# Performance work log

Measured on AMD Instinct MI355X. Metric: run time of the kernel, lower is better.

The kernel has to match this reference:

```python
import jax, jax.numpy as jnp
import numpy as np

BATCH, IN_DIM, UNITS = 65536, 256, 512

def _mask(in_dim, out_dim, density, seed):
    rng = np.random.default_rng(seed)
    return jnp.asarray((rng.random((in_dim, out_dim)) < density).astype(np.float32))

def setup_inputs() -> dict:
    key = jax.random.key(0)
    ks = jax.random.split(key, 16)
    d = {"x": jax.random.normal(ks[0], (BATCH, IN_DIM), dtype=jnp.float32)}
    # layer 0
    d["W0"] = jax.random.normal(ks[1], (IN_DIM, UNITS), dtype=jnp.float32) * 0.05
    d["b0"] = jnp.zeros((UNITS,), dtype=jnp.float32)
    d["M0"] = _mask(IN_DIM, UNITS, 0.10, 42 + 0)
    d["f0"], d["a0"], d["d0"] = jnp.float32(1.0), jnp.float32(1.0), jnp.float32(0.1)
    # layer 1 (+ skip from inputs)
    d["W1"] = jax.random.normal(ks[2], (UNITS, UNITS), dtype=jnp.float32) * 0.05
    d["b1"] = jnp.zeros((UNITS,), dtype=jnp.float32)
    d["M1"] = _mask(UNITS, UNITS, 0.10, 42 + 1)
    d["f1"], d["a1"], d["d1"] = jnp.float32(1.5), jnp.float32(1.0), jnp.float32(0.1)
    d["S1"] = jax.random.normal(ks[3], (IN_DIM, UNITS), dtype=jnp.float32) * 0.05
    d["SM1"] = _mask(IN_DIM, UNITS, 0.05, 200 + 1)
    # layer 2 (+ skip from inputs)
    d["W2"] = jax.random.normal(ks[4], (UNITS, UNITS), dtype=jnp.float32) * 0.05
    d["b2"] = jnp.zeros((UNITS,), dtype=jnp.float32)
    d["M2"] = _mask(UNITS, UNITS, 0.10, 42 + 2)
    d["f2"], d["a2"], d["d2"] = jnp.float32(2.0), jnp.float32(1.0), jnp.float32(0.1)
    d["S2"] = jax.random.normal(ks[5], (IN_DIM, UNITS), dtype=jnp.float32) * 0.05
    d["SM2"] = _mask(IN_DIM, UNITS, 0.05, 200 + 2)
    return d

def _sine(z, f, a, dec):
    # ParametricSineActivation: amplitude * sin(frequency*z) * exp(-decay*|z|)
    return a * jnp.sin(f * z) * jnp.exp(-dec * jnp.abs(z))

def reference(x, W0, b0, M0, f0, a0, d0,
              W1, b1, M1, f1, a1, d1, S1, SM1,
              W2, b2, M2, f2, a2, d2, S2, SM2):
    h0 = _sine(x @ (W0 * M0) + b0, f0, a0, d0)                       # [B, U]
    h1 = _sine(h0 @ (W1 * M1) + b1, f1, a1, d1) + x @ (S1 * SM1)     # [B, U]
    h2 = _sine(h1 @ (W2 * M2) + b2, f2, a2, d2) + x @ (S2 * SM2)     # [B, U]
    return jnp.concatenate([h0, h1, h2], axis=-1)                    # [B, 3U]
```

## Files before the change

kernel.cpp:

```cpp
#include <hip/hip_runtime.h>


#define IN_DIM 256
#define UNITS  512
#define OUTC   1536

typedef __bf16 bf16x8 __attribute__((ext_vector_type(8)));
typedef unsigned short us8 __attribute__((ext_vector_type(8)));
typedef unsigned short us4 __attribute__((ext_vector_type(4)));
typedef float f32x4 __attribute__((ext_vector_type(4)));

#define W0OFF 0
#define W1OFF 131072
#define W2OFF 393216
#define S1OFF 655360
#define S2OFF 786432

__device__ __forceinline__ unsigned short f2bf(float f) {
    unsigned u = __float_as_uint(f);
    u += 0x7FFFu + ((u >> 16) & 1u);
    return (unsigned short)(u >> 16);
}

__global__ __launch_bounds__(256) void prep_weights(
    const float* __restrict__ W0, const float* __restrict__ M0,
    const float* __restrict__ W1, const float* __restrict__ M1,
    const float* __restrict__ W2, const float* __restrict__ M2,
    const float* __restrict__ S1, const float* __restrict__ SM1,
    const float* __restrict__ S2, const float* __restrict__ SM2,
    unsigned short* __restrict__ ws)
{
    int g = blockIdx.x * 256 + threadIdx.x;
    const float* W; const float* M; int obase; int q;
    if (g < 16384)      { W = W0; M = M0;  obase = W0OFF; q = g; }
    else if (g < 49152) { W = W1; M = M1;  obase = W1OFF; q = g - 16384; }
    else if (g < 81920) { W = W2; M = M2;  obase = W2OFF; q = g - 49152; }
    else if (g < 98304) { W = S1; M = SM1; obase = S1OFF; q = g - 81920; }
    else                { W = S2; M = SM2; obase = S2OFF; q = g - 98304; }
    int frag = q >> 6, lane = q & 63;
    int kf = frag >> 5, nb = frag & 31;
    int k0 = kf * 32 + (lane >> 4) * 8;
    int n  = nb * 16 + (lane & 15);
    us8 o;
#pragma unroll
    for (int i = 0; i < 8; ++i) {
        size_t idx = (size_t)(k0 + i) * UNITS + n;
        o[i] = f2bf(W[idx] * M[idx]);
    }
    *(us8*)(ws + obase + (size_t)q * 8) = o;
}

template<int KF, int PITCH>
__device__ __forceinline__ void mm_acc(f32x4 (&acc)[2][4],
    const unsigned char* __restrict__ lsrc,
    const unsigned short* __restrict__ wfrag,
    int lane)
{
    const int lcol = lane & 15, lhi = lane >> 4;

    us8 bcur[4]; bf16x8 acur[2];
#pragma unroll
    for (int c = 0; c < 4; ++c)
        bcur[c] = *(const us8*)(wfrag + (size_t)((0 * 32 + c) * 64 + lane) * 8);
#pragma unroll
    for (int r = 0; r < 2; ++r) {
        int row = r * 16 + lcol;
        unsigned off = ((unsigned)(row * PITCH + (0 + lhi * 8) * 2)) ^ ((unsigned)((row & 7) << 4));
        acur[r] = __builtin_bit_cast(bf16x8, *(const us8*)(lsrc + off));
    }

#pragma unroll
    for (int kf = 0; kf < KF; ++kf) {
        us8 bnxt[4]; bf16x8 anxt[2];
        if (kf + 1 < KF) {
#pragma unroll
            for (int c = 0; c < 4; ++c)
                bnxt[c] = *(const us8*)(wfrag + (size_t)(((kf + 1) * 32 + c) * 64 + lane) * 8);
#pragma unroll
            for (int r = 0; r < 2; ++r) {
                int row = r * 16 + lcol;
                unsigned off = ((unsigned)(row * PITCH + ((kf + 1) * 32 + lhi * 8) * 2))
                             ^ ((unsigned)((row & 7) << 4));
                anxt[r] = __builtin_bit_cast(bf16x8, *(const us8*)(lsrc + off));
            }
        }
#pragma unroll
        for (int c = 0; c < 4; ++c) {
            bf16x8 b = __builtin_bit_cast(bf16x8, bcur[c]);
#pragma unroll
            for (int r = 0; r < 2; ++r)
                acc[r][c] = __builtin_amdgcn_mfma_f32_16x16x32_bf16(acur[r], b, acc[r][c], 0, 0, 0);
        }
        if (kf + 1 < KF) {
#pragma unroll
            for (int c = 0; c < 4; ++c) bcur[c] = bnxt[c];
#pragma unroll
            for (int r = 0; r < 2; ++r) acur[r] = anxt[r];
        }
    }
}

__device__ __forceinline__ void writeout(const unsigned char* __restrict__ hs,
                                         float* __restrict__ dst, long rb, int t)
{
    int row = t >> 4, c0 = (t & 15) * 32;
    float* o = dst + (rb + row) * OUTC + c0;
    unsigned base = (unsigned)(row * 1024 + c0 * 2);
    unsigned swz  = (unsigned)((row & 7) << 4);
#pragma unroll
    for (int i = 0; i < 4; ++i) {
        us8 v = *(const us8*)(hs + ((base + (unsigned)i * 16) ^ swz));
        f32x4 lo, hi;
#pragma unroll
        for (int j = 0; j < 4; ++j) {
            lo[j] = __uint_as_float((unsigned)v[j] << 16);
            hi[j] = __uint_as_float((unsigned)v[j + 4] << 16);
        }
        *(f32x4*)(o + i * 8)     = lo;
        *(f32x4*)(o + i * 8 + 4) = hi;
    }
}

__global__ __launch_bounds__(512, 4) void reservoir_main(
    const float* __restrict__ x,
    const unsigned short* __restrict__ wb,
    const float* __restrict__ b0, const float* __restrict__ b1, const float* __restrict__ b2,
    const float* __restrict__ pf0, const float* __restrict__ pa0, const float* __restrict__ pd0,
    const float* __restrict__ pf1, const float* __restrict__ pa1, const float* __restrict__ pd1,
    const float* __restrict__ pf2, const float* __restrict__ pa2, const float* __restrict__ pd2,
    float* __restrict__ out)
{
    __shared__ __align__(16) unsigned char lds[49152];
    unsigned char* xs = lds;
    unsigned char* hs = lds + 16384;

    const int t = threadIdx.x;
    const int wave = t >> 6, lane = t & 63;
    const int lcol = lane & 15, lhi = lane >> 4;
    const long rb = (long)blockIdx.x * 32;
    const int cb = wave * 64;
    const unsigned nb0e = (unsigned)(wave * 4) * 512;

    const float f0v = pf0[0], a0v = pa0[0], d0v = pd0[0];
    const float f1v = pf1[0], a1v = pa1[0], d1v = pd1[0];
    const float f2v = pf2[0], a2v = pa2[0], d2v = pd2[0];

    {
        int r  = t >> 4;
        int cq = (t & 15) * 4;
        const float* xp = x + (rb + r) * IN_DIM + cq;
        unsigned base = (unsigned)(r * 512 + cq * 2);
        unsigned swz  = (unsigned)((r & 7) << 4);
#pragma unroll
        for (int j = 0; j < 4; ++j) {
            f32x4 v = *(const f32x4*)(xp + j * 64);
            us4 h;
            h[0] = f2bf(v[0]); h[1] = f2bf(v[1]); h[2] = f2bf(v[2]); h[3] = f2bf(v[3]);
            *(us4*)(xs + ((base + (unsigned)j * 128) ^ swz)) = h;
        }
    }
    __syncthreads();

    f32x4 acc[2][4];

#pragma unroll
    for (int r = 0; r < 2; ++r)
#pragma unroll
        for (int c = 0; c < 4; ++c) acc[r][c] = (f32x4){0.f, 0.f, 0.f, 0.f};

    mm_acc<8, 512>(acc, xs, wb + W0OFF + nb0e, lane);

    {
        float bias[4];
#pragma unroll
        for (int c = 0; c < 4; ++c) bias[c] = b0[cb + c * 16 + lcol];
#pragma unroll
        for (int r = 0; r < 2; ++r) {
#pragma unroll
            for (int j = 0; j < 4; ++j) {
                int row = r * 16 + lhi * 4 + j;
                unsigned hswz = (unsigned)((row & 7) << 4);
#pragma unroll
                for (int c = 0; c < 4; ++c) {
                    int col = cb + c * 16 + lcol;
                    float z = acc[r][c][j] + bias[c];
                    float h = a0v * __sinf(f0v * z) * __expf(-d0v * fabsf(z));
                    *(unsigned short*)(hs + (((unsigned)(row * 1024 + col * 2)) ^ hswz)) = f2bf(h);
                }
            }
        }
    }
    __syncthreads();

    writeout(hs, out, rb, t);

#pragma unroll
    for (int r = 0; r < 2; ++r)
#pragma unroll
        for (int c = 0; c < 4; ++c) acc[r][c] = (f32x4){0.f, 0.f, 0.f, 0.f};

    mm_acc<16, 1024>(acc, hs, wb + W1OFF + nb0e, lane);

    {
        float bias[4];
#pragma unroll
        for (int c = 0; c < 4; ++c) bias[c] = b1[cb + c * 16 + lcol];
#pragma unroll
        for (int c = 0; c < 4; ++c) {
#pragma unroll
            for (int r = 0; r < 2; ++r) {
#pragma unroll
                for (int j = 0; j < 4; ++j) {
                    float z = acc[r][c][j] + bias[c];
                    acc[r][c][j] = a1v * __sinf(f1v * z) * __expf(-d1v * fabsf(z));
                }
            }
        }
    }
    mm_acc<8, 512>(acc, xs, wb + S1OFF + nb0e, lane);
    __syncthreads();

#pragma unroll
    for (int r = 0; r < 2; ++r) {
#pragma unroll
        for (int j = 0; j < 4; ++j) {
            int row = r * 16 + lhi * 4 + j;
            unsigned hswz = (unsigned)((row & 7) << 4);
#pragma unroll
            for (int c = 0; c < 4; ++c) {
                int col = cb + c * 16 + lcol;
                *(unsigned short*)(hs + (((unsigned)(row * 1024 + col * 2)) ^ hswz)) = f2bf(acc[r][c][j]);
            }
        }
    }
    __syncthreads();

    writeout(hs, out + UNITS, rb, t);

#pragma unroll
    for (int r = 0; r < 2; ++r)
#pragma unroll
        for (int c = 0; c < 4; ++c) acc[r][c] = (f32x4){0.f, 0.f, 0.f, 0.f};

    mm_acc<16, 1024>(acc, hs, wb + W2OFF + nb0e, lane);

    {
        float bias[4];
#pragma unroll
        for (int c = 0; c < 4; ++c) bias[c] = b2[cb + c * 16 + lcol];
#pragma unroll
        for (int c = 0; c < 4; ++c) {
#pragma unroll
            for (int r = 0; r < 2; ++r) {
#pragma unroll
                for (int j = 0; j < 4; ++j) {
                    float z = acc[r][c][j] + bias[c];
                    acc[r][c][j] = a2v * __sinf(f2v * z) * __expf(-d2v * fabsf(z));
                }
            }
        }
    }
    mm_acc<8, 512>(acc, xs, wb + S2OFF + nb0e, lane);
    __syncthreads();

#pragma unroll
    for (int r = 0; r < 2; ++r) {
#pragma unroll
        for (int j = 0; j < 4; ++j) {
            int row = r * 16 + lhi * 4 + j;
            unsigned hswz = (unsigned)((row & 7) << 4);
#pragma unroll
            for (int c = 0; c < 4; ++c) {
                int col = cb + c * 16 + lcol;
                *(unsigned short*)(hs + (((unsigned)(row * 1024 + col * 2)) ^ hswz)) = f2bf(acc[r][c][j]);
            }
        }
    }
    __syncthreads();

    writeout(hs, out + 2 * UNITS, rb, t);
}

extern "C" void kernel_launch(void* const* d_in, const int* in_sizes, int n_in,
                              void* d_out, int out_size, void* d_ws, size_t ws_size,
                              hipStream_t stream)
{
    (void)in_sizes; (void)n_in; (void)out_size; (void)ws_size;
    const float* x   = (const float*)d_in[0];
    const float* W0  = (const float*)d_in[1];
    const float* b0  = (const float*)d_in[2];
    const float* M0  = (const float*)d_in[3];
    const float* f0  = (const float*)d_in[4];
    const float* a0  = (const float*)d_in[5];
    const float* d0  = (const float*)d_in[6];
    const float* W1  = (const float*)d_in[7];
    const float* b1  = (const float*)d_in[8];
    const float* M1  = (const float*)d_in[9];
    const float* f1  = (const float*)d_in[10];
    const float* a1  = (const float*)d_in[11];
    const float* d1  = (const float*)d_in[12];
    const float* S1  = (const float*)d_in[13];
    const float* SM1 = (const float*)d_in[14];
    const float* W2  = (const float*)d_in[15];
    const float* b2  = (const float*)d_in[16];
    const float* M2  = (const float*)d_in[17];
    const float* f2  = (const float*)d_in[18];
    const float* a2  = (const float*)d_in[19];
    const float* d2  = (const float*)d_in[20];
    const float* S2  = (const float*)d_in[21];
    const float* SM2 = (const float*)d_in[22];

    unsigned short* wb = (unsigned short*)d_ws;
    float* out = (float*)d_out;

    prep_weights<<<448, 256, 0, stream>>>(W0, M0, W1, M1, W2, M2, S1, SM1, S2, SM2, wb);
    reservoir_main<<<65536 / 32, 512, 0, stream>>>(x, wb, b0, b1, b2,
                                                   f0, a0, d0, f1, a1, d1, f2, a2, d2, out);
}
```

Before: 769.0 us.

## Double row tile to 64 per block and deepen fragment prefetch to two stages

Each block now processes 64 batch rows instead of 32. Each wave accumulates a 4x4 grid of MFMA tiles, so every weight fragment loaded from global memory feeds twice as many MFMAs, which halves weight traffic per row. The k-loop prefetch is deepened from one to two stages to hide load latency. In exchange, LDS use doubles to 96KB, accumulator registers double, and launch bounds drop to 2 blocks per CU, which lowers occupancy and halves the grid size.

```diff
diff --git a/kernel.cpp b/kernel.cpp
--- a/kernel.cpp
+++ b/kernel.cpp
@@ -51,77 +51,71 @@
 }
 
 template<int KF, int PITCH>
-__device__ __forceinline__ void mm_acc(f32x4 (&acc)[2][4],
+__device__ __forceinline__ void mm_acc(f32x4 (&acc)[4][4],
     const unsigned char* __restrict__ lsrc,
     const unsigned short* __restrict__ wfrag,
     int lane)
 {
     const int lcol = lane & 15, lhi = lane >> 4;
 
-    us8 bcur[4]; bf16x8 acur[2];
-#pragma unroll
-    for (int c = 0; c < 4; ++c)
-        bcur[c] = *(const us8*)(wfrag + (size_t)((0 * 32 + c) * 64 + lane) * 8);
-#pragma unroll
-    for (int r = 0; r < 2; ++r) {
-        int row = r * 16 + lcol;
-        unsigned off = ((unsigned)(row * PITCH + (0 + lhi * 8) * 2)) ^ ((unsigned)((row & 7) << 4));
-        acur[r] = __builtin_bit_cast(bf16x8, *(const us8*)(lsrc + off));
-    }
+#define LOADB(dst, kk) { _Pragma("unroll") \
+    for (int c_ = 0; c_ < 4; ++c_) \
+        dst[c_] = *(const us8*)(wfrag + (size_t)(((kk) * 32 + c_) * 64 + lane) * 8); }
+#define LOADA(dst, kk) { _Pragma("unroll") \
+    for (int r_ = 0; r_ < 4; ++r_) { \
+        int row_ = r_ * 16 + lcol; \
+        unsigned off_ = ((unsigned)(row_ * PITCH + ((kk) * 32 + lhi * 8) * 2)) \
+                      ^ ((unsigned)((row_ & 7) << 4)); \
+        dst[r_] = __builtin_bit_cast(bf16x8, *(const us8*)(lsrc + off_)); } }
+
+    us8 bc[4], bn[4]; bf16x8 ac[4], an[4];
+    LOADB(bc, 0); LOADA(ac, 0);
+    if (KF > 1) { LOADB(bn, 1); LOADA(an, 1); }
 
 #pragma unroll
     for (int kf = 0; kf < KF; ++kf) {
-        us8 bnxt[4]; bf16x8 anxt[2];
-        if (kf + 1 < KF) {
-#pragma unroll
-            for (int c = 0; c < 4; ++c)
-                bnxt[c] = *(const us8*)(wfrag + (size_t)(((kf + 1) * 32 + c) * 64 + lane) * 8);
-#pragma unroll
-            for (int r = 0; r < 2; ++r) {
-                int row = r * 16 + lcol;
-                unsigned off = ((unsigned)(row * PITCH + ((kf + 1) * 32 + lhi * 8) * 2))
-                             ^ ((unsigned)((row & 7) << 4));
-                anxt[r] = __builtin_bit_cast(bf16x8, *(const us8*)(lsrc + off));
-            }
-        }
+        us8 bf_[4]; bf16x8 af_[4];
+        if (kf + 2 < KF) { LOADB(bf_, kf + 2); LOADA(af_, kf + 2); }
 #pragma unroll
         for (int c = 0; c < 4; ++c) {
-            bf16x8 b = __builtin_bit_cast(bf16x8, bcur[c]);
-#pragma unroll
-            for (int r = 0; r < 2; ++r)
-                acc[r][c] = __builtin_amdgcn_mfma_f32_16x16x32_bf16(acur[r], b, acc[r][c], 0, 0, 0);
-        }
-        if (kf + 1 < KF) {
-#pragma unroll
-            for (int c = 0; c < 4; ++c) bcur[c] = bnxt[c];
-#pragma unroll
-            for (int r = 0; r < 2; ++r) acur[r] = anxt[r];
-        }
-    }
+            bf16x8 b = __builtin_bit_cast(bf16x8, bc[c]);
+#pragma unroll
+            for (int r = 0; r < 4; ++r)
+                acc[r][c] = __builtin_amdgcn_mfma_f32_16x16x32_bf16(ac[r], b, acc[r][c], 0, 0, 0);
+        }
+#pragma unroll
+        for (int i = 0; i < 4; ++i) { bc[i] = bn[i]; ac[i] = an[i]; bn[i] = bf_[i]; an[i] = af_[i]; }
+    }
+#undef LOADB
+#undef LOADA
 }
 
 __device__ __forceinline__ void writeout(const unsigned char* __restrict__ hs,
                                          float* __restrict__ dst, long rb, int t)
 {
-    int row = t >> 4, c0 = (t & 15) * 32;
-    float* o = dst + (rb + row) * OUTC + c0;
-    unsigned base = (unsigned)(row * 1024 + c0 * 2);
-    unsigned swz  = (unsigned)((row & 7) << 4);
-#pragma unroll
-    for (int i = 0; i < 4; ++i) {
-        us8 v = *(const us8*)(hs + ((base + (unsigned)i * 16) ^ swz));
-        f32x4 lo, hi;
-#pragma unroll
-        for (int j = 0; j < 4; ++j) {
-            lo[j] = __uint_as_float((unsigned)v[j] << 16);
-            hi[j] = __uint_as_float((unsigned)v[j + 4] << 16);
-        }
-        *(f32x4*)(o + i * 8)     = lo;
-        *(f32x4*)(o + i * 8 + 4) = hi;
-    }
-}
-
-__global__ __launch_bounds__(512, 4) void reservoir_main(
+#pragma unroll
+    for (int half = 0; half < 2; ++half) {
+        int row = (t >> 4) + half * 32;
+        int c0 = (t & 15) * 32;
+        float* o = dst + (rb + row) * OUTC + c0;
+        unsigned base = (unsigned)(row * 1024 + c0 * 2);
+        unsigned swz  = (unsigned)((row & 7) << 4);
+#pragma unroll
+        for (int i = 0; i < 4; ++i) {
+            us8 v = *(const us8*)(hs + ((base + (unsigned)i * 16) ^ swz));
+            f32x4 lo, hi;
+#pragma unroll
+            for (int j = 0; j < 4; ++j) {
+                lo[j] = __uint_as_float((unsigned)v[j] << 16);
+                hi[j] = __uint_as_float((unsigned)v[j + 4] << 16);
+            }
+            *(f32x4*)(o + i * 8)     = lo;
+            *(f32x4*)(o + i * 8 + 4) = hi;
+        }
+    }
+}
+
+__global__ __launch_bounds__(512, 2) void reservoir_main(
     const float* __restrict__ x,
     const unsigned short* __restrict__ wb,
     const float* __restrict__ b0, const float* __restrict__ b1, const float* __restrict__ b2,
@@ -130,14 +124,14 @@
     const float* __restrict__ pf2, const float* __restrict__ pa2, const float* __restrict__ pd2,
     float* __restrict__ out)
 {
-    __shared__ __align__(16) unsigned char lds[49152];
+    __shared__ __align__(16) unsigned char lds[98304];
     unsigned char* xs = lds;
-    unsigned char* hs = lds + 16384;
+    unsigned char* hs = lds + 32768;
 
     const int t = threadIdx.x;
     const int wave = t >> 6, lane = t & 63;
     const int lcol = lane & 15, lhi = lane >> 4;
-    const long rb = (long)blockIdx.x * 32;
+    const long rb = (long)blockIdx.x * 64;
     const int cb = wave * 64;
     const unsigned nb0e = (unsigned)(wave * 4) * 512;
 
@@ -146,25 +140,25 @@
     const float f2v = pf2[0], a2v = pa2[0], d2v = pd2[0];
 
     {
-        int r  = t >> 4;
-        int cq = (t & 15) * 4;
+        int r  = t >> 3;
+        int cq = (t & 7) * 4;
         const float* xp = x + (rb + r) * IN_DIM + cq;
         unsigned base = (unsigned)(r * 512 + cq * 2);
         unsigned swz  = (unsigned)((r & 7) << 4);
 #pragma unroll
-        for (int j = 0; j < 4; ++j) {
-            f32x4 v = *(const f32x4*)(xp + j * 64);
+        for (int j = 0; j < 8; ++j) {
+            f32x4 v = *(const f32x4*)(xp + j * 32);
             us4 h;
             h[0] = f2bf(v[0]); h[1] = f2bf(v[1]); h[2] = f2bf(v[2]); h[3] = f2bf(v[3]);
-            *(us4*)(xs + ((base + (unsigned)j * 128) ^ swz)) = h;
-        }
-    }
-    __syncthreads();
-
-    f32x4 acc[2][4];
-
-#pragma unroll
-    for (int r = 0; r < 2; ++r)
+            *(us4*)(xs + ((base + (unsigned)j * 64) ^ swz)) = h;
+        }
+    }
+    __syncthreads();
+
+    f32x4 acc[4][4];
+
+#pragma unroll
+    for (int r = 0; r < 4; ++r)
 #pragma unroll
         for (int c = 0; c < 4; ++c) acc[r][c] = (f32x4){0.f, 0.f, 0.f, 0.f};
 
@@ -175,7 +169,7 @@
 #pragma unroll
         for (int c = 0; c < 4; ++c) bias[c] = b0[cb + c * 16 + lcol];
 #pragma unroll
-        for (int r = 0; r < 2; ++r) {
+        for (int r = 0; r < 4; ++r) {
 #pragma unroll
             for (int j = 0; j < 4; ++j) {
                 int row = r * 16 + lhi * 4 + j;
@@ -195,7 +189,7 @@
     writeout(hs, out, rb, t);
 
 #pragma unroll
-    for (int r = 0; r < 2; ++r)
+    for (int r = 0; r < 4; ++r)
 #pragma unroll
         for (int c = 0; c < 4; ++c) acc[r][c] = (f32x4){0.f, 0.f, 0.f, 0.f};
 
@@ -208,7 +202,7 @@
 #pragma unroll
         for (int c = 0; c < 4; ++c) {
 #pragma unroll
-            for (int r = 0; r < 2; ++r) {
+            for (int r = 0; r < 4; ++r) {
 #pragma unroll
                 for (int j = 0; j < 4; ++j) {
                     float z = acc[r][c][j] + bias[c];
@@ -221,7 +215,7 @@
     __syncthreads();
 
 #pragma unroll
-    for (int r = 0; r < 2; ++r) {
+    for (int r = 0; r < 4; ++r) {
 #pragma unroll
         for (int j = 0; j < 4; ++j) {
             int row = r * 16 + lhi * 4 + j;
@@ -238,7 +232,7 @@
     writeout(hs, out + UNITS, rb, t);
 
 #pragma unroll
-    for (int r = 0; r < 2; ++r)
+    for (int r = 0; r < 4; ++r)
 #pragma unroll
         for (int c = 0; c < 4; ++c) acc[r][c] = (f32x4){0.f, 0.f, 0.f, 0.f};
 
@@ -251,7 +245,7 @@
 #pragma unroll
         for (int c = 0; c < 4; ++c) {
 #pragma unroll
-            for (int r = 0; r < 2; ++r) {
+            for (int r = 0; r < 4; ++r) {
 #pragma unroll
                 for (int j = 0; j < 4; ++j) {
                     float z = acc[r][c][j] + bias[c];
@@ -264,7 +258,7 @@
     __syncthreads();
 
 #pragma unroll
-    for (int r = 0; r < 2; ++r) {
+    for (int r = 0; r < 4; ++r) {
 #pragma unroll
         for (int j = 0; j < 4; ++j) {
             int row = r * 16 + lhi * 4 + j;
@@ -314,6 +308,6 @@
     float* out = (float*)d_out;
 
     prep_weights<<<448, 256, 0, stream>>>(W0, M0, W1, M1, W2, M2, S1, SM1, S2, SM2, wb);
-    reservoir_main<<<65536 / 32, 512, 0, stream>>>(x, wb, b0, b1, b2,
+    reservoir_main<<<65536 / 64, 512, 0, stream>>>(x, wb, b0, b1, b2,
                                                    f0, a0, d0, f1, a1, d1, f2, a2, d2, out);
 }
```

Result: slower. 792.8 us (+3.1%).
